# Performance work log

Hardware: AMD Instinct MI355X
Metric: run time of the kernel (lower is better)

## Reference

```python
import jax, jax.numpy as jnp
import numpy as np

D_MODEL = 1024
N_HEADS = 16
HEAD_DIM = D_MODEL // N_HEADS


def setup_inputs() -> dict:
    key = jax.random.key(0)
    k_x, k_wqkv, k_bqkv, k_wo, k_bo = jax.random.split(key, 5)
    b, t = 4, 2048
    s = 1.0 / np.sqrt(D_MODEL)
    return {
        "x": jax.random.normal(k_x, (b, t, D_MODEL), dtype=jnp.float32),
        "w_qkv": jax.random.uniform(k_wqkv, (D_MODEL, 3 * D_MODEL), jnp.float32, -s, s),
        "b_qkv": jax.random.uniform(k_bqkv, (3 * D_MODEL,), jnp.float32, -s, s),
        "w_out": jax.random.uniform(k_wo, (D_MODEL, D_MODEL), jnp.float32, -s, s),
        "b_out": jax.random.uniform(k_bo, (D_MODEL,), jnp.float32, -s, s),
    }


def reference(x, w_qkv, b_qkv, w_out, b_out):
    b, t, _ = x.shape
    # fused QKV projection -> [b, t, 3, h, d] -> q,k,v each [b, h, t, d]
    qkv = (x @ w_qkv + b_qkv).reshape(b, t, 3, N_HEADS, HEAD_DIM)
    q, k, v = jnp.moveaxis(qkv, 2, 0)          # each [b, t, h, d]
    q = q.transpose(0, 2, 1, 3)                # [b, h, t, d]
    k = k.transpose(0, 2, 1, 3)
    v = v.transpose(0, 2, 1, 3)
    scale = 1.0 / np.sqrt(HEAD_DIM).astype(np.float32)
    logits = jnp.einsum('bhqd,bhkd->bhqk', q, k) * scale
    causal = jnp.tril(jnp.ones((t, t), dtype=bool))
    logits = jnp.where(causal, logits, jnp.finfo(logits.dtype).min)
    attn = jax.nn.softmax(logits, axis=-1)
    out = jnp.einsum('bhqk,bhkd->bhqd', attn, v)      # [b, h, t, d]
    out = out.transpose(0, 2, 1, 3).reshape(b, t, D_MODEL)
    return out @ w_out + b_out
```

## Files before the change

kernel.cpp:

```cpp
#include <hip/hip_runtime.h>
#include <hip/hip_bf16.h>
#include <math.h>

#define NHEADS 16
#define HDIM   64
#define SEQT   2048
#define NBATCH 4
#define DMODEL 1024
#define MROWS  (NBATCH * SEQT)

typedef __bf16 bf16;
typedef bf16  bf16x8 __attribute__((ext_vector_type(8)));
typedef float f32x4  __attribute__((ext_vector_type(4)));

#define MFMA_BF16(a, b, c) __builtin_amdgcn_mfma_f32_16x16x32_bf16((a), (b), (c), 0, 0, 0)

__device__ __forceinline__ void gload_lds16(const void* g, void* l) {
  __builtin_amdgcn_global_load_lds((const __attribute__((address_space(1))) void*)g,
                                   (__attribute__((address_space(3))) void*)l, 16, 0, 0);
}


__global__ __launch_bounds__(256) void k_cvt_f32_bf16(const float* __restrict__ in,
                                                      bf16* __restrict__ out, int n8) {
  int i = blockIdx.x * blockDim.x + threadIdx.x;
  if (i >= n8) return;
  const float4* in4 = (const float4*)in;
  float4 a = in4[(size_t)i * 2], b = in4[(size_t)i * 2 + 1];
  bf16x8 v;
  v[0] = (bf16)a.x; v[1] = (bf16)a.y; v[2] = (bf16)a.z; v[3] = (bf16)a.w;
  v[4] = (bf16)b.x; v[5] = (bf16)b.y; v[6] = (bf16)b.z; v[7] = (bf16)b.w;
  *(bf16x8*)(out + (size_t)i * 8) = v;
}

__global__ __launch_bounds__(256) void k_transpose_f32_bf16(const float* __restrict__ in,
                                                            bf16* __restrict__ out,
                                                            int R, int C) {
  int nct = C >> 6;
  int rt = blockIdx.x / nct, ct = blockIdx.x % nct;
  __shared__ float tile[64][65];
  int tid = threadIdx.x;
#pragma unroll
  for (int i = 0; i < 16; i++) {
    int e = i * 256 + tid, r = e >> 6, c = e & 63;
    tile[r][c] = in[(size_t)(rt * 64 + r) * C + ct * 64 + c];
  }
  __syncthreads();
#pragma unroll
  for (int i = 0; i < 16; i++) {
    int e = i * 256 + tid, r = e >> 6, c = e & 63;
    out[(size_t)(ct * 64 + r) * R + rt * 64 + c] = (bf16)tile[c][r];
  }
}

__global__ __launch_bounds__(256) void k_transpose_v(const bf16* __restrict__ v,
                                                     bf16* __restrict__ vt) {
  int tt = blockIdx.x & 31;
  int bh = blockIdx.x >> 5;
  __shared__ bf16 tile[64][65];
  int tid = threadIdx.x;
  const bf16* src = v + (size_t)bh * SEQT * 64 + (size_t)tt * 64 * 64;
#pragma unroll
  for (int i = 0; i < 16; i++) {
    int e = i * 256 + tid, r = e >> 6, c = e & 63;
    tile[r][c] = src[r * 64 + c];
  }
  __syncthreads();
  bf16* dst = vt + (size_t)bh * 64 * SEQT + tt * 64;
#pragma unroll
  for (int i = 0; i < 16; i++) {
    int e = i * 256 + tid, r = e >> 6, c = e & 63;
    dst[(size_t)r * SEQT + c] = tile[c][r];
  }
}


__device__ __forceinline__ void gemm128_core(const bf16* __restrict__ A,
                                             const bf16* __restrict__ Bt,
                                             int K, int bm, int bn, char* smem,
                                             f32x4 (&acc)[4][4]) {
  int tid = threadIdx.x, lane = tid & 63, w = tid >> 6;
  int l15 = lane & 15, g = lane >> 4;
  int wrow = (w >> 1) * 64, wcol = (w & 1) * 64;
  char* As = smem;
  char* Bs = smem + 8192;
  const char* Ag = (const char*)(A + (size_t)bm * 128 * K);
  const char* Bg = (const char*)(Bt + (size_t)bn * 128 * K);
  const int rowB = K * 2;
  int srow = w * 16 + (lane >> 2);
  int scol = (lane & 3) * 16;

  for (int kt = 0; kt < K / 32; kt++) {
#pragma unroll
    for (int is = 0; is < 2; is++) {
      int row = is * 64 + srow;
      gload_lds16(Ag + (size_t)row * rowB + kt * 64 + scol, As + is * 4096 + w * 1024);
      gload_lds16(Bg + (size_t)row * rowB + kt * 64 + scol, Bs + is * 4096 + w * 1024);
    }
    __syncthreads();
    bf16x8 af[4], bfr[4];
#pragma unroll
    for (int i = 0; i < 4; i++)
      af[i] = *(const bf16x8*)&As[(wrow + i * 16 + l15) * 64 + g * 16];
#pragma unroll
    for (int j = 0; j < 4; j++)
      bfr[j] = *(const bf16x8*)&Bs[(wcol + j * 16 + l15) * 64 + g * 16];
#pragma unroll
    for (int i = 0; i < 4; i++)
#pragma unroll
      for (int j = 0; j < 4; j++)
        acc[i][j] = MFMA_BF16(af[i], bfr[j], acc[i][j]);
    __syncthreads();
  }
}

__global__ __launch_bounds__(256) void k_gemm_qkv(const bf16* __restrict__ A,
                                                  const bf16* __restrict__ Bt,
                                                  const float* __restrict__ bias,
                                                  bf16* __restrict__ Qo,
                                                  bf16* __restrict__ Ko,
                                                  bf16* __restrict__ Vo) {
  const int K = DMODEL, NB = 24;
  int bm = blockIdx.x / NB, bn = blockIdx.x % NB;
  __shared__ __align__(16) char smem[16384];
  f32x4 acc[4][4] = {};
  gemm128_core(A, Bt, K, bm, bn, smem, acc);

  int tid = threadIdx.x, lane = tid & 63, w = tid >> 6;
  int l15 = lane & 15, g = lane >> 4;
  int wrow = (w >> 1) * 64, wcol = (w & 1) * 64;
  int rowbase = bm * 128 + wrow;
  int b = (bm * 128) >> 11;
#pragma unroll
  for (int j = 0; j < 4; j++) {
    int n = bn * 128 + wcol + j * 16 + l15;
    float bj = bias[n];
    int which = n >> 10;
    int nn = n & 1023;
    int head = nn >> 6, d = nn & 63;
    bf16* dst = (which == 0) ? Qo : (which == 1) ? Ko : Vo;
    size_t base = ((size_t)(b * NHEADS + head) * SEQT) * 64 + d;
#pragma unroll
    for (int i = 0; i < 4; i++) {
#pragma unroll
      for (int r = 0; r < 4; r++) {
        int row = rowbase + i * 16 + g * 4 + r;
        int t = row & (SEQT - 1);
        dst[base + (size_t)t * 64] = (bf16)(acc[i][j][r] + bj);
      }
    }
  }
}

__global__ __launch_bounds__(256) void k_gemm_out(const bf16* __restrict__ A,
                                                  const bf16* __restrict__ Bt,
                                                  const float* __restrict__ bias,
                                                  float* __restrict__ C) {
  const int K = DMODEL, NB = 8;
  int bm = blockIdx.x / NB, bn = blockIdx.x % NB;
  __shared__ __align__(16) char smem[16384];
  f32x4 acc[4][4] = {};
  gemm128_core(A, Bt, K, bm, bn, smem, acc);

  int tid = threadIdx.x, lane = tid & 63, w = tid >> 6;
  int l15 = lane & 15, g = lane >> 4;
  int wrow = (w >> 1) * 64, wcol = (w & 1) * 64;
#pragma unroll
  for (int j = 0; j < 4; j++) {
    int n = bn * 128 + wcol + j * 16 + l15;
    float bj = bias[n];
#pragma unroll
    for (int i = 0; i < 4; i++) {
#pragma unroll
      for (int r = 0; r < 4; r++) {
        int row = bm * 128 + wrow + i * 16 + g * 4 + r;
        C[(size_t)row * DMODEL + n] = acc[i][j][r] + bj;
      }
    }
  }
}


__global__ __launch_bounds__(256) void k_attn(const bf16* __restrict__ Q,
                                              const bf16* __restrict__ Kg,
                                              const bf16* __restrict__ VT,
                                              bf16* __restrict__ Oo) {
  int bh = blockIdx.x & 63;
  int qi = 31 - (blockIdx.x >> 6);
  int tid = threadIdx.x, lane = tid & 63, w = tid >> 6;
  int l15 = lane & 15, g = lane >> 4;
  __shared__ __align__(16) char smem[40960];
  char* Ps = smem + 32768 + w * 2048;

  const bf16* Qbh = Q  + (size_t)bh * SEQT * 64;
  const char* Kbyte = (const char*)(Kg + (size_t)bh * SEQT * 64);
  const char* Vbyte = (const char*)(VT + (size_t)bh * 64 * SEQT);
  int qlo = qi * 64 + w * 16;

  int pA = w * 1024 + lane * 16;
  int pB = pA + 4096;
  int rA = pA >> 7, rB = pB >> 7;
  int lgA = pA ^ ((rA & 7) << 4), lgB = pB ^ ((rB & 7) << 4);
  int vA = rA * 4096 + (lgA & 127), vB = rB * 4096 + (lgB & 127);
  int dstA = w * 1024, dstB = 4096 + w * 1024;

  bf16x8 aq[2];
#pragma unroll
  for (int ks = 0; ks < 2; ks++) {
    bf16x8 v = *(const bf16x8*)(Qbh + (size_t)(qlo + l15) * 64 + ks * 32 + g * 8);
#pragma unroll
    for (int e = 0; e < 8; e++) v[e] = (bf16)((float)v[e] * 0.125f);
    aq[ks] = v;
  }

  float m[4], lsum[4];
  f32x4 o[4];
#pragma unroll
  for (int r = 0; r < 4; r++) { m[r] = -INFINITY; lsum[r] = 0.f; }
#pragma unroll
  for (int jd = 0; jd < 4; jd++) o[jd] = (f32x4){0.f, 0.f, 0.f, 0.f};

  {
    gload_lds16(Kbyte + lgA, smem + dstA);
    gload_lds16(Kbyte + lgB, smem + dstB);
    gload_lds16(Vbyte + vA, smem + 16384 + dstA);
    gload_lds16(Vbyte + vB, smem + 16384 + dstB);
  }

  int cur = 0;
  for (int j = 0; j <= qi; j++) {
    __syncthreads();
    if (j < qi) {
      int nx = cur ^ 1;
      const char* kg = Kbyte + (size_t)(j + 1) * 8192;
      const char* vg = Vbyte + (size_t)(j + 1) * 128;
      gload_lds16(kg + lgA, smem + nx * 8192 + dstA);
      gload_lds16(kg + lgB, smem + nx * 8192 + dstB);
      gload_lds16(vg + vA, smem + 16384 + nx * 8192 + dstA);
      gload_lds16(vg + vB, smem + 16384 + nx * 8192 + dstB);
    }
    char* Ks = smem + cur * 8192;
    char* Vs = smem + 16384 + cur * 8192;

    f32x4 s[4];
#pragma unroll
    for (int c = 0; c < 4; c++) {
      int row = c * 16 + l15;
      f32x4 t = {0.f, 0.f, 0.f, 0.f};
      t = MFMA_BF16(aq[0], *(const bf16x8*)&Ks[(row * 128 + 0  + g * 16) ^ ((l15 & 7) << 4)], t);
      t = MFMA_BF16(aq[1], *(const bf16x8*)&Ks[(row * 128 + 64 + g * 16) ^ ((l15 & 7) << 4)], t);
      s[c] = t;
    }

    bool diag = (j == qi);
    int qrb = w * 16 + g * 4;
    float mx[4];
#pragma unroll
    for (int r = 0; r < 4; r++) {
      float v0 = -INFINITY;
#pragma unroll
      for (int c = 0; c < 4; c++) {
        float v = s[c][r];
        if (diag && (c * 16 + l15) > (qrb + r)) { v = -INFINITY; s[c][r] = v; }
        v0 = fmaxf(v0, v);
      }
      v0 = fmaxf(v0, __shfl_xor(v0, 1));
      v0 = fmaxf(v0, __shfl_xor(v0, 2));
      v0 = fmaxf(v0, __shfl_xor(v0, 4));
      v0 = fmaxf(v0, __shfl_xor(v0, 8));
      mx[r] = v0;
    }

    bool need = (mx[0] > m[0] + 8.f) | (mx[1] > m[1] + 8.f) |
                (mx[2] > m[2] + 8.f) | (mx[3] > m[3] + 8.f);
    if (__any(need)) {
#pragma unroll
      for (int r = 0; r < 4; r++) {
        float mn = fmaxf(m[r], mx[r]);
        float co = __expf(m[r] - mn);
        m[r] = mn;
        lsum[r] *= co;
#pragma unroll
        for (int jd = 0; jd < 4; jd++) o[jd][r] *= co;
      }
    }

#pragma unroll
    for (int r = 0; r < 4; r++) {
      float ssum = 0.f;
#pragma unroll
      for (int c = 0; c < 4; c++) {
        float p = __expf(s[c][r] - m[r]);
        s[c][r] = p;
        ssum += p;
      }
      ssum += __shfl_xor(ssum, 1);
      ssum += __shfl_xor(ssum, 2);
      ssum += __shfl_xor(ssum, 4);
      ssum += __shfl_xor(ssum, 8);
      lsum[r] += ssum;
    }

#pragma unroll
    for (int c = 0; c < 4; c++) {
#pragma unroll
      for (int r = 0; r < 4; r++) {
        int row = g * 4 + r;
        int addr = (row * 128 + (c * 16 + l15) * 2) ^ ((row & 7) << 4);
        *(bf16*)&Ps[addr] = (bf16)s[c][r];
      }
    }

#pragma unroll
    for (int ks = 0; ks < 2; ks++) {
      bf16x8 pa = *(const bf16x8*)&Ps[(l15 * 128 + ks * 64 + g * 16) ^ ((l15 & 7) << 4)];
#pragma unroll
      for (int jd = 0; jd < 4; jd++) {
        int vrow = jd * 16 + l15;
        bf16x8 bv = *(const bf16x8*)&Vs[(vrow * 128 + ks * 64 + g * 16) ^ ((l15 & 7) << 4)];
        o[jd] = MFMA_BF16(pa, bv, o[jd]);
      }
    }
    cur ^= 1;
  }

  int b = bh >> 4, h = bh & 15;
#pragma unroll
  for (int jd = 0; jd < 4; jd++) {
#pragma unroll
    for (int r = 0; r < 4; r++) {
      int t = qlo + g * 4 + r;
      float vv = o[jd][r] / lsum[r];
      Oo[((size_t)(b * SEQT + t)) * DMODEL + h * 64 + jd * 16 + l15] = (bf16)vv;
    }
  }
}


extern "C" void kernel_launch(void* const* d_in, const int* in_sizes, int n_in,
                              void* d_out, int out_size, void* d_ws, size_t ws_size,
                              hipStream_t stream) {
  const float* x     = (const float*)d_in[0];
  const float* w_qkv = (const float*)d_in[1];
  const float* b_qkv = (const float*)d_in[2];
  const float* w_out = (const float*)d_in[3];
  const float* b_out = (const float*)d_in[4];
  float* out = (float*)d_out;

  char* ws = (char*)d_ws;
  bf16* xb    = (bf16*)(ws);
  bf16* wqkvT = (bf16*)(ws + (16u << 20));
  bf16* woutT = (bf16*)(ws + (22u << 20));
  bf16* Qb    = (bf16*)(ws + (24u << 20));
  bf16* Kb    = (bf16*)(ws + (40u << 20));
  bf16* Vb    = (bf16*)(ws + (56u << 20));
  bf16* VTb   = (bf16*)(ws + (72u << 20));
  bf16* attn_o = xb;

  k_cvt_f32_bf16<<<(MROWS * DMODEL / 8 + 255) / 256, 256, 0, stream>>>(x, xb, MROWS * DMODEL / 8);
  k_transpose_f32_bf16<<<16 * 48, 256, 0, stream>>>(w_qkv, wqkvT, DMODEL, 3 * DMODEL);
  k_transpose_f32_bf16<<<16 * 16, 256, 0, stream>>>(w_out, woutT, DMODEL, DMODEL);
  k_gemm_qkv<<<64 * 24, 256, 0, stream>>>(xb, wqkvT, b_qkv, Qb, Kb, Vb);
  k_transpose_v<<<64 * 32, 256, 0, stream>>>(Vb, VTb);
  k_attn<<<32 * 64, 256, 0, stream>>>(Qb, Kb, VTb, attn_o);
  k_gemm_out<<<64 * 8, 256, 0, stream>>>(attn_o, woutT, b_out, out);
}
```

Baseline: 306.8 us.

## Rewrite attention with 32x32 MFMA, transposed scores, register-resident P

The attention kernel now uses 32x32x16 bf16 MFMA and computes S^T (K as A operand, Q as B operand), so each lane owns one query row. Softmax row statistics then need only a single cross-half shuffle. P is packed to bf16 with v_cvt_pk and rearranged with v_permlane32_swap instead of going through LDS. Each block now covers 128 query rows (32 per wave) instead of 64, halving the grid and reusing each K/V tile across more queries, at the cost of more registers and skipped-tile imbalance near the diagonal.

```diff
diff --git a/kernel.cpp b/kernel.cpp
--- a/kernel.cpp
+++ b/kernel.cpp
@@ -12,12 +12,25 @@
 typedef __bf16 bf16;
 typedef bf16  bf16x8 __attribute__((ext_vector_type(8)));
 typedef float f32x4  __attribute__((ext_vector_type(4)));
+typedef float f32x16 __attribute__((ext_vector_type(16)));
+typedef unsigned int u32x4 __attribute__((ext_vector_type(4)));
 
 #define MFMA_BF16(a, b, c) __builtin_amdgcn_mfma_f32_16x16x32_bf16((a), (b), (c), 0, 0, 0)
+#define MFMA32(a, b, c)    __builtin_amdgcn_mfma_f32_32x32x16_bf16((a), (b), (c), 0, 0, 0)
+#define Z16 {0.f,0.f,0.f,0.f,0.f,0.f,0.f,0.f,0.f,0.f,0.f,0.f,0.f,0.f,0.f,0.f}
 
 __device__ __forceinline__ void gload_lds16(const void* g, void* l) {
   __builtin_amdgcn_global_load_lds((const __attribute__((address_space(1))) void*)g,
                                    (__attribute__((address_space(3))) void*)l, 16, 0, 0);
+}
+
+__device__ __forceinline__ unsigned cvtpk_bf16(float lo, float hi) {
+  unsigned r;
+  asm("v_cvt_pk_bf16_f32 %0, %1, %2" : "=v"(r) : "v"(lo), "v"(hi));
+  return r;
+}
+__device__ __forceinline__ void plswap(unsigned& a, unsigned& b) {
+  asm volatile("v_permlane32_swap_b32 %0, %1" : "+v"(a), "+v"(b));
 }
 
 
@@ -186,153 +199,148 @@
                                               const bf16* __restrict__ VT,
                                               bf16* __restrict__ Oo) {
   int bh = blockIdx.x & 63;
-  int qi = 31 - (blockIdx.x >> 6);
-  int tid = threadIdx.x, lane = tid & 63, w = tid >> 6;
-  int l15 = lane & 15, g = lane >> 4;
-  __shared__ __align__(16) char smem[40960];
-  char* Ps = smem + 32768 + w * 2048;
-
-  const bf16* Qbh = Q  + (size_t)bh * SEQT * 64;
+  int qi = 15 - (blockIdx.x >> 6);
+  int tid = threadIdx.x, lane = tid & 63, wv = tid >> 6;
+  int l31 = lane & 31, hi = lane >> 5;
+  __shared__ __align__(16) char smem[32768];
+
+  const bf16* Qbh = Q + (size_t)bh * SEQT * 64;
   const char* Kbyte = (const char*)(Kg + (size_t)bh * SEQT * 64);
   const char* Vbyte = (const char*)(VT + (size_t)bh * 64 * SEQT);
-  int qlo = qi * 64 + w * 16;
-
-  int pA = w * 1024 + lane * 16;
-  int pB = pA + 4096;
+  int qbase = qi * 128 + wv * 32;
+  int ql = qbase + l31;
+
+  int pA = tid * 16, pB = pA + 4096;
   int rA = pA >> 7, rB = pB >> 7;
   int lgA = pA ^ ((rA & 7) << 4), lgB = pB ^ ((rB & 7) << 4);
   int vA = rA * 4096 + (lgA & 127), vB = rB * 4096 + (lgB & 127);
-  int dstA = w * 1024, dstB = 4096 + w * 1024;
-
-  bf16x8 aq[2];
-#pragma unroll
-  for (int ks = 0; ks < 2; ks++) {
-    bf16x8 v = *(const bf16x8*)(Qbh + (size_t)(qlo + l15) * 64 + ks * 32 + g * 8);
+
+  bf16x8 qf[4];
+#pragma unroll
+  for (int s = 0; s < 4; s++) {
+    bf16x8 v = *(const bf16x8*)(Qbh + (size_t)ql * 64 + s * 16 + hi * 8);
 #pragma unroll
     for (int e = 0; e < 8; e++) v[e] = (bf16)((float)v[e] * 0.125f);
-    aq[ks] = v;
-  }
-
-  float m[4], lsum[4];
-  f32x4 o[4];
-#pragma unroll
-  for (int r = 0; r < 4; r++) { m[r] = -INFINITY; lsum[r] = 0.f; }
-#pragma unroll
-  for (int jd = 0; jd < 4; jd++) o[jd] = (f32x4){0.f, 0.f, 0.f, 0.f};
-
-  {
-    gload_lds16(Kbyte + lgA, smem + dstA);
-    gload_lds16(Kbyte + lgB, smem + dstB);
-    gload_lds16(Vbyte + vA, smem + 16384 + dstA);
-    gload_lds16(Vbyte + vB, smem + 16384 + dstB);
-  }
-
-  int cur = 0;
-  for (int j = 0; j <= qi; j++) {
+    qf[s] = v;
+  }
+
+  float m = -INFINITY, lsum = 0.f;
+  f32x16 o[2] = {Z16, Z16};
+
+  gload_lds16(Kbyte + lgA, smem + pA);
+  gload_lds16(Kbyte + lgB, smem + pB);
+  gload_lds16(Vbyte + vA, smem + 16384 + pA);
+  gload_lds16(Vbyte + vB, smem + 16384 + pB);
+
+  int NT = 2 * qi + 2, cur = 0;
+  for (int j = 0; j < NT; j++) {
     __syncthreads();
-    if (j < qi) {
+    if (j + 1 < NT) {
       int nx = cur ^ 1;
       const char* kg = Kbyte + (size_t)(j + 1) * 8192;
       const char* vg = Vbyte + (size_t)(j + 1) * 128;
-      gload_lds16(kg + lgA, smem + nx * 8192 + dstA);
-      gload_lds16(kg + lgB, smem + nx * 8192 + dstB);
-      gload_lds16(vg + vA, smem + 16384 + nx * 8192 + dstA);
-      gload_lds16(vg + vB, smem + 16384 + nx * 8192 + dstB);
-    }
-    char* Ks = smem + cur * 8192;
-    char* Vs = smem + 16384 + cur * 8192;
-
-    f32x4 s[4];
-#pragma unroll
-    for (int c = 0; c < 4; c++) {
-      int row = c * 16 + l15;
-      f32x4 t = {0.f, 0.f, 0.f, 0.f};
-      t = MFMA_BF16(aq[0], *(const bf16x8*)&Ks[(row * 128 + 0  + g * 16) ^ ((l15 & 7) << 4)], t);
-      t = MFMA_BF16(aq[1], *(const bf16x8*)&Ks[(row * 128 + 64 + g * 16) ^ ((l15 & 7) << 4)], t);
-      s[c] = t;
-    }
-
-    bool diag = (j == qi);
-    int qrb = w * 16 + g * 4;
-    float mx[4];
-#pragma unroll
-    for (int r = 0; r < 4; r++) {
-      float v0 = -INFINITY;
-#pragma unroll
-      for (int c = 0; c < 4; c++) {
-        float v = s[c][r];
-        if (diag && (c * 16 + l15) > (qrb + r)) { v = -INFINITY; s[c][r] = v; }
-        v0 = fmaxf(v0, v);
-      }
-      v0 = fmaxf(v0, __shfl_xor(v0, 1));
-      v0 = fmaxf(v0, __shfl_xor(v0, 2));
-      v0 = fmaxf(v0, __shfl_xor(v0, 4));
-      v0 = fmaxf(v0, __shfl_xor(v0, 8));
-      mx[r] = v0;
-    }
-
-    bool need = (mx[0] > m[0] + 8.f) | (mx[1] > m[1] + 8.f) |
-                (mx[2] > m[2] + 8.f) | (mx[3] > m[3] + 8.f);
-    if (__any(need)) {
-#pragma unroll
-      for (int r = 0; r < 4; r++) {
-        float mn = fmaxf(m[r], mx[r]);
-        float co = __expf(m[r] - mn);
-        m[r] = mn;
-        lsum[r] *= co;
-#pragma unroll
-        for (int jd = 0; jd < 4; jd++) o[jd][r] *= co;
-      }
-    }
-
-#pragma unroll
-    for (int r = 0; r < 4; r++) {
-      float ssum = 0.f;
-#pragma unroll
-      for (int c = 0; c < 4; c++) {
-        float p = __expf(s[c][r] - m[r]);
-        s[c][r] = p;
-        ssum += p;
-      }
-      ssum += __shfl_xor(ssum, 1);
-      ssum += __shfl_xor(ssum, 2);
-      ssum += __shfl_xor(ssum, 4);
-      ssum += __shfl_xor(ssum, 8);
-      lsum[r] += ssum;
-    }
-
-#pragma unroll
-    for (int c = 0; c < 4; c++) {
-#pragma unroll
-      for (int r = 0; r < 4; r++) {
-        int row = g * 4 + r;
-        int addr = (row * 128 + (c * 16 + l15) * 2) ^ ((row & 7) << 4);
-        *(bf16*)&Ps[addr] = (bf16)s[c][r];
-      }
-    }
-
-#pragma unroll
-    for (int ks = 0; ks < 2; ks++) {
-      bf16x8 pa = *(const bf16x8*)&Ps[(l15 * 128 + ks * 64 + g * 16) ^ ((l15 & 7) << 4)];
-#pragma unroll
-      for (int jd = 0; jd < 4; jd++) {
-        int vrow = jd * 16 + l15;
-        bf16x8 bv = *(const bf16x8*)&Vs[(vrow * 128 + ks * 64 + g * 16) ^ ((l15 & 7) << 4)];
-        o[jd] = MFMA_BF16(pa, bv, o[jd]);
+      gload_lds16(kg + lgA, smem + nx * 8192 + pA);
+      gload_lds16(kg + lgB, smem + nx * 8192 + pB);
+      gload_lds16(vg + vA, smem + 16384 + nx * 8192 + pA);
+      gload_lds16(vg + vB, smem + 16384 + nx * 8192 + pB);
+    }
+    if (j * 64 <= qbase + 31) {
+      const char* Ks = smem + cur * 8192;
+      const char* Vs = smem + 16384 + cur * 8192;
+
+      f32x16 st[2];
+#pragma unroll
+      for (int h = 0; h < 2; h++) {
+        f32x16 acc = Z16;
+#pragma unroll
+        for (int s = 0; s < 4; s++) {
+          int row = h * 32 + l31;
+          bf16x8 kf = *(const bf16x8*)&Ks[(row * 128 + s * 32 + hi * 16) ^ ((l31 & 7) << 4)];
+          acc = MFMA32(kf, qf[s], acc);
+        }
+        st[h] = acc;
+      }
+
+      if (j * 64 + 63 > qbase) {
+        int rel = ql - (j * 64 + 4 * hi);
+#pragma unroll
+        for (int r = 0; r < 16; r++) {
+          const int R0 = (r & 3) + 8 * (r >> 2);
+          if (R0 > rel) st[0][r] = -INFINITY;
+          if (R0 > rel - 32) st[1][r] = -INFINITY;
+        }
+      }
+
+      float m0 = -INFINITY, m1 = -INFINITY, m2 = -INFINITY, m3 = -INFINITY;
+#pragma unroll
+      for (int h = 0; h < 2; h++)
+#pragma unroll
+        for (int r = 0; r < 16; r += 4) {
+          m0 = fmaxf(m0, st[h][r]);
+          m1 = fmaxf(m1, st[h][r + 1]);
+          m2 = fmaxf(m2, st[h][r + 2]);
+          m3 = fmaxf(m3, st[h][r + 3]);
+        }
+      float mx = fmaxf(fmaxf(m0, m1), fmaxf(m2, m3));
+      mx = fmaxf(mx, __shfl_xor(mx, 32));
+
+      if (__any(mx > m + 8.f)) {
+        float mn = fmaxf(m, mx), co = __expf(m - mn);
+        m = mn; lsum *= co;
+#pragma unroll
+        for (int r = 0; r < 16; r++) {
+          const int R0 = (r & 3) + 8 * (r >> 2);
+          float fac = __shfl(co, R0 + 4 * hi);
+          o[0][r] *= fac; o[1][r] *= fac;
+        }
+      }
+
+      float s0 = 0.f, s1 = 0.f, s2 = 0.f, s3 = 0.f;
+#pragma unroll
+      for (int h = 0; h < 2; h++)
+#pragma unroll
+        for (int r = 0; r < 16; r += 4) {
+          float p0 = __expf(st[h][r] - m);     st[h][r] = p0;     s0 += p0;
+          float p1 = __expf(st[h][r + 1] - m); st[h][r + 1] = p1; s1 += p1;
+          float p2 = __expf(st[h][r + 2] - m); st[h][r + 2] = p2; s2 += p2;
+          float p3 = __expf(st[h][r + 3] - m); st[h][r + 3] = p3; s3 += p3;
+        }
+      lsum += (s0 + s1) + (s2 + s3);
+
+#pragma unroll
+      for (int h = 0; h < 2; h++) {
+        unsigned pw[8];
+#pragma unroll
+        for (int i = 0; i < 8; i++) pw[i] = cvtpk_bf16(st[h][2 * i], st[h][2 * i + 1]);
+        plswap(pw[0], pw[2]); plswap(pw[1], pw[3]);
+        plswap(pw[4], pw[6]); plswap(pw[5], pw[7]);
+        u32x4 f0 = {pw[0], pw[1], pw[2], pw[3]};
+        u32x4 f1 = {pw[4], pw[5], pw[6], pw[7]};
+        bf16x8 pa0 = __builtin_bit_cast(bf16x8, f0);
+        bf16x8 pa1 = __builtin_bit_cast(bf16x8, f1);
+#pragma unroll
+        for (int dh = 0; dh < 2; dh++) {
+          int vrow = dh * 32 + l31;
+          bf16x8 bv0 = *(const bf16x8*)&Vs[(vrow * 128 + (2 * h) * 32 + hi * 16) ^ ((l31 & 7) << 4)];
+          bf16x8 bv1 = *(const bf16x8*)&Vs[(vrow * 128 + (2 * h + 1) * 32 + hi * 16) ^ ((l31 & 7) << 4)];
+          o[dh] = MFMA32(pa0, bv0, o[dh]);
+          o[dh] = MFMA32(pa1, bv1, o[dh]);
+        }
       }
     }
     cur ^= 1;
   }
 
-  int b = bh >> 4, h = bh & 15;
-#pragma unroll
-  for (int jd = 0; jd < 4; jd++) {
-#pragma unroll
-    for (int r = 0; r < 4; r++) {
-      int t = qlo + g * 4 + r;
-      float vv = o[jd][r] / lsum[r];
-      Oo[((size_t)(b * SEQT + t)) * DMODEL + h * 64 + jd * 16 + l15] = (bf16)vv;
-    }
+  float inv = 1.f / (lsum + __shfl_xor(lsum, 32));
+  int b = bh >> 4, hd = bh & 15;
+#pragma unroll
+  for (int r = 0; r < 16; r++) {
+    const int R0 = (r & 3) + 8 * (r >> 2);
+    float fac = __shfl(inv, R0 + 4 * hi);
+    int qrow = qbase + R0 + 4 * hi;
+    size_t off = ((size_t)(b * SEQT + qrow)) * DMODEL + hd * 64;
+    Oo[off + l31]      = (bf16)(o[0][r] * fac);
+    Oo[off + 32 + l31] = (bf16)(o[1][r] * fac);
   }
 }
 
@@ -362,6 +370,6 @@
   k_transpose_f32_bf16<<<16 * 16, 256, 0, stream>>>(w_out, woutT, DMODEL, DMODEL);
   k_gemm_qkv<<<64 * 24, 256, 0, stream>>>(xb, wqkvT, b_qkv, Qb, Kb, Vb);
   k_transpose_v<<<64 * 32, 256, 0, stream>>>(Vb, VTb);
-  k_attn<<<32 * 64, 256, 0, stream>>>(Qb, Kb, VTb, attn_o);
+  k_attn<<<16 * 64, 256, 0, stream>>>(Qb, Kb, VTb, attn_o);
   k_gemm_out<<<64 * 8, 256, 0, stream>>>(attn_o, woutT, b_out, out);
 }
```

Measured after the change: 261.7 us. 14.7% less time.
